# Optimization experiments

Measured on AMD Instinct MI355X. Metric: run time of the kernel, lower is better.

The kernel has to match this reference:

```python
import jax, jax.numpy as jnp
import numpy as np

D_MODEL = 1024
N_HEADS = 8
HEAD_DIM = D_MODEL // N_HEADS
B, T = 4, 2048


def setup_inputs() -> dict:
    key = jax.random.key(0)
    ks = jax.random.split(key, 10)
    x = jax.random.normal(ks[0], (B, T, D_MODEL), dtype=jnp.float32)
    # causal mask: True entries are masked (matches torch masked_fill semantics)
    mask = jnp.triu(jnp.ones((T, T), dtype=bool), k=1)

    def xavier(k, shape):
        fan_in, fan_out = shape[1], shape[0]
        lim = float(np.sqrt(6.0 / (fan_in + fan_out)))
        return jax.random.uniform(k, shape, jnp.float32, -lim, lim)

    Wq = xavier(ks[1], (D_MODEL, D_MODEL)); bq = jnp.zeros((D_MODEL,), jnp.float32)
    Wk = xavier(ks[2], (D_MODEL, D_MODEL)); bk = jnp.zeros((D_MODEL,), jnp.float32)
    Wv = xavier(ks[3], (D_MODEL, D_MODEL)); bv = jnp.zeros((D_MODEL,), jnp.float32)
    Wo = xavier(ks[4], (D_MODEL, D_MODEL)); bo = jnp.zeros((D_MODEL,), jnp.float32)
    return {"x": x, "mask": mask, "Wq": Wq, "bq": bq, "Wk": Wk, "bk": bk,
            "Wv": Wv, "bv": bv, "Wo": Wo, "bo": bo}


def reference(x, mask, Wq, bq, Wk, bk, Wv, bv, Wo, bo):
    Bsz, Tlen, _ = x.shape
    # torch Linear: y = x @ W.T + b
    Q = (x @ Wq.T + bq).reshape(Bsz, Tlen, N_HEADS, HEAD_DIM).transpose(0, 2, 1, 3)  # [B,H,T,Dh]
    K = (x @ Wk.T + bk).reshape(Bsz, Tlen, N_HEADS, HEAD_DIM).transpose(0, 2, 1, 3)  # [B,H,T,Dh]
    V_shared = x @ Wv.T + bv  # [B,T,D] shared across heads
    scale = 1.0 / jnp.sqrt(jnp.float32(HEAD_DIM))
    scores = jnp.einsum('bhqd,bhkd->bhqk', Q, K) * scale  # [B,H,T,T]
    scores = jnp.where(mask[None, None, :, :], jnp.float32(-1e9), scores)
    attn_per_head = jax.nn.softmax(scores, axis=-1)
    alpha_agg = attn_per_head.mean(axis=1)  # [B,T,T] head-averaged attention
    out = jnp.einsum('bqk,bkd->bqd', alpha_agg, V_shared) @ Wo.T + bo
    return out, alpha_agg
```

## Files before the change

kernel.cpp:

```cpp
#include <hip/hip_runtime.h>
#include <hip/hip_bf16.h>

#define D_MODEL 1024
#define NH 8
#define HD 128
#define BATCH 4
#define TSEQ 2048
#define MROWS (BATCH * TSEQ)

typedef __attribute__((ext_vector_type(8))) __bf16 bf16x8;
typedef __attribute__((ext_vector_type(4))) __bf16 bf16x4;
typedef __attribute__((ext_vector_type(4))) float f32x4;
typedef __attribute__((ext_vector_type(8))) unsigned short u16x8;

#define SC2 0.1275174441680632f

__device__ __forceinline__ void gload16(const void* g, void* lds) {
  __builtin_amdgcn_global_load_lds(
      (const __attribute__((address_space(1))) unsigned int*)g,
      (__attribute__((address_space(3))) unsigned int*)lds, 16, 0, 0);
}

__global__ __launch_bounds__(256) void cvt_f32_to_bf16(const float* __restrict__ in,
                                                       __bf16* __restrict__ out, int n4) {
  int i = blockIdx.x * 256 + threadIdx.x;
  if (i < n4) {
    float4 v = reinterpret_cast<const float4*>(in)[i];
    bf16x4 o;
    o[0] = (__bf16)v.x; o[1] = (__bf16)v.y; o[2] = (__bf16)v.z; o[3] = (__bf16)v.w;
    reinterpret_cast<bf16x4*>(out)[i] = o;
  }
}

__global__ __launch_bounds__(256) void cvt4_weights(const float* __restrict__ w0,
                                                    const float* __restrict__ w1,
                                                    const float* __restrict__ w2,
                                                    const float* __restrict__ w3,
                                                    __bf16* __restrict__ out) {
  const int per = D_MODEL * D_MODEL / 4;
  int i = blockIdx.x * 256 + threadIdx.x;
  int m = i / per, j = i - m * per;
  const float* src = (m == 0) ? w0 : (m == 1) ? w1 : (m == 2) ? w2 : w3;
  float4 v = reinterpret_cast<const float4*>(src)[j];
  bf16x4 o;
  o[0] = (__bf16)v.x; o[1] = (__bf16)v.y; o[2] = (__bf16)v.z; o[3] = (__bf16)v.w;
  reinterpret_cast<bf16x4*>(out)[i] = o;
}

template <bool BF16OUT, bool CAUSAL, bool AFP32>
__global__ __launch_bounds__(256) void gemm128(const void* __restrict__ Aip,
                                               const __bf16* __restrict__ Bp,
                                               const float* __restrict__ bias,
                                               void* __restrict__ Yp, int K, int ldy,
                                               size_t sA, size_t sB, size_t sY) {
  __shared__ __bf16 As[2][128 * 32];
  __shared__ __bf16 Bs[2][128 * 32];
  const int tid = threadIdx.x;
  const int w = tid >> 6, l = tid & 63;
  const int lr = l & 15, lg = l >> 4;
  const int m0 = blockIdx.y * 128, n0 = blockIdx.x * 128;
  const int z = blockIdx.z;
  const __bf16* Ab = AFP32 ? nullptr : (const __bf16*)Aip + z * sA;
  const float* Af = AFP32 ? (const float*)Aip + z * sA : nullptr;
  const __bf16* Bb = Bp + z * sB;
  const int wm = w >> 1, wn = w & 1;
  f32x4 acc[4][4] = {};
  const int Klim = CAUSAL ? (m0 + 128 < K ? m0 + 128 : K) : K;
  const int nt = Klim >> 5;

  auto stage = [&](int t, int buf) {
    const int k0 = t << 5;
    if constexpr (!AFP32) {
#pragma unroll
      for (int i = 0; i < 2; ++i) {
        int s = w * 128 + i * 64 + l;
        int row = s >> 2, scp = s & 3;
        int sc = scp ^ ((row >> 1) & 3);
        gload16(Ab + (size_t)(m0 + row) * K + k0 + sc * 8, (char*)As[buf] + s * 16);
      }
    } else {
#pragma unroll
      for (int i = 0; i < 2; ++i) {
        int s = w * 128 + i * 64 + l;
        int row = s >> 2, sc = s & 3;
        const float* src = Af + (size_t)(m0 + row) * K + k0 + sc * 8;
        float4 lo = *reinterpret_cast<const float4*>(src);
        float4 hi = *reinterpret_cast<const float4*>(src + 4);
        bf16x8 v;
        v[0] = (__bf16)lo.x; v[1] = (__bf16)lo.y; v[2] = (__bf16)lo.z; v[3] = (__bf16)lo.w;
        v[4] = (__bf16)hi.x; v[5] = (__bf16)hi.y; v[6] = (__bf16)hi.z; v[7] = (__bf16)hi.w;
        int p = row * 4 + (sc ^ ((row >> 1) & 3));
        *reinterpret_cast<bf16x8*>((char*)As[buf] + p * 16) = v;
      }
    }
#pragma unroll
    for (int i = 0; i < 2; ++i) {
      int s = w * 128 + i * 64 + l;
      int row = s >> 2, scp = s & 3;
      int sc = scp ^ ((row >> 1) & 3);
      gload16(Bb + (size_t)(n0 + row) * K + k0 + sc * 8, (char*)Bs[buf] + s * 16);
    }
  };

  stage(0, 0);
  __syncthreads();
  int cur = 0;
  for (int t = 0; t < nt; ++t) {
    if (t + 1 < nt) stage(t + 1, cur ^ 1);
    bf16x8 af[4], bf[4];
#pragma unroll
    for (int f = 0; f < 4; ++f) {
      int ar = wm * 64 + f * 16 + lr;
      af[f] = *reinterpret_cast<const bf16x8*>((const char*)As[cur] + ar * 64 +
                                               ((lg ^ ((ar >> 1) & 3)) * 16));
      int br = wn * 64 + f * 16 + lr;
      bf[f] = *reinterpret_cast<const bf16x8*>((const char*)Bs[cur] + br * 64 +
                                               ((lg ^ ((br >> 1) & 3)) * 16));
    }
#pragma unroll
    for (int mf = 0; mf < 4; ++mf)
#pragma unroll
      for (int nf = 0; nf < 4; ++nf)
        acc[mf][nf] = __builtin_amdgcn_mfma_f32_16x16x32_bf16(af[mf], bf[nf], acc[mf][nf], 0, 0, 0);
    __syncthreads();
    cur ^= 1;
  }

#pragma unroll
  for (int mf = 0; mf < 4; ++mf) {
#pragma unroll
    for (int nf = 0; nf < 4; ++nf) {
#pragma unroll
      for (int r = 0; r < 4; ++r) {
        int grow = m0 + wm * 64 + mf * 16 + lg * 4 + r;
        int gcol = n0 + wn * 64 + nf * 16 + lr;
        float v = acc[mf][nf][r];
        if (bias) v += bias[gcol];
        if constexpr (BF16OUT)
          ((__bf16*)Yp + z * sY)[(size_t)grow * ldy + gcol] = (__bf16)v;
        else
          ((float*)Yp + z * sY)[(size_t)grow * ldy + gcol] = v;
      }
    }
  }
}

__global__ __launch_bounds__(256) void transpose_v(const __bf16* __restrict__ V,
                                                   __bf16* __restrict__ Vt) {
  __shared__ unsigned short tile[64 * 72];
  const int b = blockIdx.z;
  const int t0 = blockIdx.x * 64, d0 = blockIdx.y * 64;
  const int tid = threadIdx.x;
#pragma unroll
  for (int i = 0; i < 2; ++i) {
    int s = i * 256 + tid;
    int r = s >> 3, c8 = s & 7;
    u16x8 v = *reinterpret_cast<const u16x8*>(V + ((size_t)b * TSEQ + t0 + r) * D_MODEL + d0 + c8 * 8);
    *reinterpret_cast<u16x8*>(&tile[r * 72 + c8 * 8]) = v;
  }
  __syncthreads();
#pragma unroll
  for (int i = 0; i < 2; ++i) {
    int s = i * 256 + tid;
    int dr = s >> 3, t8 = s & 7;
    u16x8 o;
#pragma unroll
    for (int j = 0; j < 8; ++j) o[j] = tile[(t8 * 8 + j) * 72 + dr];
    *reinterpret_cast<u16x8*>(Vt + ((size_t)b * D_MODEL + d0 + dr) * TSEQ + t0 + t8 * 8) = o;
  }
}

#define STAGE_T(srcbase, dst)                                                      \
  {                                                                                \
    _Pragma("unroll") for (int i = 0; i < 4; ++i) {                                \
      int s = i * 256 + tid;                                                       \
      int row = s >> 4, sp = s & 15;                                               \
      int sl = sp ^ (row & 15);                                                    \
      gload16((srcbase) + (size_t)row * D_MODEL + sl * 8, (char*)(dst) + s * 16);  \
    }                                                                              \
  }

__device__ __forceinline__ bf16x8 ldfrag(const __bf16* t, int row, int c, int lg) {
  return *reinterpret_cast<const bf16x8*>((const char*)t + row * 256 +
                                          (((c * 4 + lg) ^ (row & 15)) * 16));
}

__global__ __launch_bounds__(256) void attn_stats(const __bf16* __restrict__ Q,
                                                  const __bf16* __restrict__ Kp,
                                                  float* __restrict__ Linv) {
  __shared__ __bf16 Qs[64 * 128];
  __shared__ __bf16 Ks[2][64 * 128];
  __shared__ float Lred[2][64];
  const int tid = threadIdx.x;
  const int w = tid >> 6, l = tid & 63;
  const int lr = l & 15, lg = l >> 4;
  const int wq = w >> 1, wk = w & 1;
  const int qt = blockIdx.x, q0 = qt * 64;
  const int b = blockIdx.y >> 3, h = blockIdx.y & 7;

  const __bf16* qsrc = Q + ((size_t)(b * TSEQ + q0)) * D_MODEL + h * HD;
  const __bf16* kbase = Kp + ((size_t)b * TSEQ) * D_MODEL + h * HD;
  STAGE_T(qsrc, Qs);
  STAGE_T(kbase, Ks[0]);
  __syncthreads();

  bf16x8 af[2][4];
#pragma unroll
  for (int mf = 0; mf < 2; ++mf)
#pragma unroll
    for (int c = 0; c < 4; ++c) af[mf][c] = ldfrag(Qs, wq * 32 + mf * 16 + lr, c, lg);

  float lsum[2][4] = {};
  int cur = 0;
  for (int kt = 0; kt <= qt; ++kt) {
    if (kt < qt) STAGE_T(kbase + (size_t)(kt + 1) * 64 * D_MODEL, Ks[cur ^ 1]);
    bf16x8 bfr[2][4];
#pragma unroll
    for (int nf = 0; nf < 2; ++nf)
#pragma unroll
      for (int c = 0; c < 4; ++c) bfr[nf][c] = ldfrag(Ks[cur], wk * 32 + nf * 16 + lr, c, lg);
    f32x4 acc[2][2] = {};
#pragma unroll
    for (int c = 0; c < 4; ++c)
#pragma unroll
      for (int mf = 0; mf < 2; ++mf)
#pragma unroll
        for (int nf = 0; nf < 2; ++nf)
          acc[mf][nf] = __builtin_amdgcn_mfma_f32_16x16x32_bf16(af[mf][c], bfr[nf][c], acc[mf][nf], 0, 0, 0);
    if (kt == qt) {
#pragma unroll
      for (int mf = 0; mf < 2; ++mf)
#pragma unroll
        for (int nf = 0; nf < 2; ++nf)
#pragma unroll
          for (int r = 0; r < 4; ++r) {
            int q = q0 + wq * 32 + mf * 16 + lg * 4 + r;
            int k = kt * 64 + wk * 32 + nf * 16 + lr;
            if (k <= q) lsum[mf][r] += exp2f(acc[mf][nf][r] * SC2);
          }
    } else {
#pragma unroll
      for (int mf = 0; mf < 2; ++mf)
#pragma unroll
        for (int nf = 0; nf < 2; ++nf)
#pragma unroll
          for (int r = 0; r < 4; ++r) lsum[mf][r] += exp2f(acc[mf][nf][r] * SC2);
    }
    __syncthreads();
    cur ^= 1;
  }
#pragma unroll
  for (int m = 1; m < 16; m <<= 1)
#pragma unroll
    for (int mf = 0; mf < 2; ++mf)
#pragma unroll
      for (int r = 0; r < 4; ++r) lsum[mf][r] += __shfl_xor(lsum[mf][r], m, 64);
  if (lr == 0) {
#pragma unroll
    for (int mf = 0; mf < 2; ++mf)
#pragma unroll
      for (int r = 0; r < 4; ++r) Lred[wk][wq * 32 + mf * 16 + lg * 4 + r] = lsum[mf][r];
  }
  __syncthreads();
  if (tid < 64) {
    float s = Lred[0][tid] + Lred[1][tid];
    Linv[((size_t)(b * NH + h)) * TSEQ + q0 + tid] = 1.0f / (8.0f * s);
  }
}

__global__ __launch_bounds__(256) void attn_alpha(const __bf16* __restrict__ Q,
                                                  const __bf16* __restrict__ Kp,
                                                  const float* __restrict__ Linv,
                                                  float* __restrict__ alpha) {
  const int kt = blockIdx.x, qt = blockIdx.y, b = blockIdx.z;
  const int q0 = qt * 64, k0 = kt * 64;
  const int tid = threadIdx.x;
  if (kt > qt) {
    float4 zz = {0.f, 0.f, 0.f, 0.f};
#pragma unroll
    for (int i = 0; i < 4; ++i) {
      int s = i * 256 + tid;
      int row = s >> 4, c4 = s & 15;
      *reinterpret_cast<float4*>(alpha + ((size_t)(b * TSEQ) + q0 + row) * TSEQ + k0 + c4 * 4) = zz;
    }
    return;
  }
  __shared__ __bf16 Qs[2][64 * 128];
  __shared__ __bf16 Ks[2][64 * 128];
  const int w = tid >> 6, l = tid & 63;
  const int lr = l & 15, lg = l >> 4;
  const int wq = w >> 1, wk = w & 1;
  const __bf16* qb0 = Q + ((size_t)(b * TSEQ + q0)) * D_MODEL;
  const __bf16* kb0 = Kp + ((size_t)(b * TSEQ + k0)) * D_MODEL;
  float outv[2][2][4] = {};

  STAGE_T(qb0, Qs[0]);
  STAGE_T(kb0, Ks[0]);
  __syncthreads();
  int cur = 0;
  for (int h = 0; h < NH; ++h) {
    if (h + 1 < NH) {
      STAGE_T(qb0 + (h + 1) * HD, Qs[cur ^ 1]);
      STAGE_T(kb0 + (h + 1) * HD, Ks[cur ^ 1]);
    }
    bf16x8 af[2][4], bfr[2][4];
#pragma unroll
    for (int mf = 0; mf < 2; ++mf)
#pragma unroll
      for (int c = 0; c < 4; ++c) af[mf][c] = ldfrag(Qs[cur], wq * 32 + mf * 16 + lr, c, lg);
#pragma unroll
    for (int nf = 0; nf < 2; ++nf)
#pragma unroll
      for (int c = 0; c < 4; ++c) bfr[nf][c] = ldfrag(Ks[cur], wk * 32 + nf * 16 + lr, c, lg);
    f32x4 acc[2][2] = {};
#pragma unroll
    for (int c = 0; c < 4; ++c)
#pragma unroll
      for (int mf = 0; mf < 2; ++mf)
#pragma unroll
        for (int nf = 0; nf < 2; ++nf)
          acc[mf][nf] = __builtin_amdgcn_mfma_f32_16x16x32_bf16(af[mf][c], bfr[nf][c], acc[mf][nf], 0, 0, 0);
    float4 li[2];
#pragma unroll
    for (int mf = 0; mf < 2; ++mf)
      li[mf] = *reinterpret_cast<const float4*>(
          &Linv[((size_t)(b * NH + h)) * TSEQ + q0 + wq * 32 + mf * 16 + lg * 4]);
    if (kt == qt) {
#pragma unroll
      for (int mf = 0; mf < 2; ++mf)
#pragma unroll
        for (int nf = 0; nf < 2; ++nf)
#pragma unroll
          for (int r = 0; r < 4; ++r) {
            int q = q0 + wq * 32 + mf * 16 + lg * 4 + r;
            int k = k0 + wk * 32 + nf * 16 + lr;
            if (k <= q)
              outv[mf][nf][r] += exp2f(acc[mf][nf][r] * SC2) * (&li[mf].x)[r];
          }
    } else {
#pragma unroll
      for (int mf = 0; mf < 2; ++mf)
#pragma unroll
        for (int nf = 0; nf < 2; ++nf)
#pragma unroll
          for (int r = 0; r < 4; ++r)
            outv[mf][nf][r] += exp2f(acc[mf][nf][r] * SC2) * (&li[mf].x)[r];
    }
    __syncthreads();
    cur ^= 1;
  }
#pragma unroll
  for (int mf = 0; mf < 2; ++mf)
#pragma unroll
    for (int nf = 0; nf < 2; ++nf)
#pragma unroll
      for (int r = 0; r < 4; ++r)
        alpha[((size_t)(b * TSEQ) + q0 + wq * 32 + mf * 16 + lg * 4 + r) * TSEQ +
              k0 + wk * 32 + nf * 16 + lr] = outv[mf][nf][r];
}

extern "C" void kernel_launch(void* const* d_in, const int* in_sizes, int n_in,
                              void* d_out, int out_size, void* d_ws, size_t ws_size,
                              hipStream_t stream) {
  const float* x  = (const float*)d_in[0];
  const float* Wq = (const float*)d_in[2];
  const float* bq = (const float*)d_in[3];
  const float* Wk = (const float*)d_in[4];
  const float* bk = (const float*)d_in[5];
  const float* Wv = (const float*)d_in[6];
  const float* bv = (const float*)d_in[7];
  const float* Wo = (const float*)d_in[8];
  const float* bo = (const float*)d_in[9];

  float* out_f = (float*)d_out;
  float* alpha = out_f + (size_t)MROWS * D_MODEL;

  char* p = (char*)d_ws;
  __bf16* xb  = (__bf16*)p; p += (size_t)MROWS * D_MODEL * 2;
  __bf16* wqb = (__bf16*)p; p += (size_t)D_MODEL * D_MODEL * 2;
  __bf16* wkb = (__bf16*)p; p += (size_t)D_MODEL * D_MODEL * 2;
  __bf16* wvb = (__bf16*)p; p += (size_t)D_MODEL * D_MODEL * 2;
  __bf16* wob = (__bf16*)p; p += (size_t)D_MODEL * D_MODEL * 2;
  __bf16* qb  = (__bf16*)p; p += (size_t)MROWS * D_MODEL * 2;
  __bf16* kb  = (__bf16*)p; p += (size_t)MROWS * D_MODEL * 2;
  __bf16* vb  = (__bf16*)p; p += (size_t)MROWS * D_MODEL * 2;
  __bf16* vtb = (__bf16*)p; p += (size_t)BATCH * D_MODEL * TSEQ * 2;
  float* linv = (float*)p;  p += (size_t)BATCH * NH * TSEQ * 4;
  __bf16* midb = xb;

  {
    int n4 = MROWS * D_MODEL / 4;
    cvt_f32_to_bf16<<<n4 / 256, 256, 0, stream>>>(x, xb, n4);
    int w4 = 4 * D_MODEL * D_MODEL / 4;
    cvt4_weights<<<w4 / 256, 256, 0, stream>>>(Wq, Wk, Wv, Wo, wqb);
  }

  dim3 pgrid(D_MODEL / 128, MROWS / 128, 1);
  gemm128<true, false, false><<<pgrid, 256, 0, stream>>>(xb, wqb, bq, qb, D_MODEL, D_MODEL, 0, 0, 0);
  gemm128<true, false, false><<<pgrid, 256, 0, stream>>>(xb, wkb, bk, kb, D_MODEL, D_MODEL, 0, 0, 0);
  gemm128<true, false, false><<<pgrid, 256, 0, stream>>>(xb, wvb, bv, vb, D_MODEL, D_MODEL, 0, 0, 0);

  transpose_v<<<dim3(TSEQ / 64, D_MODEL / 64, BATCH), 256, 0, stream>>>(vb, vtb);

  attn_stats<<<dim3(TSEQ / 64, BATCH * NH), 256, 0, stream>>>(qb, kb, linv);

  attn_alpha<<<dim3(TSEQ / 64, TSEQ / 64, BATCH), 256, 0, stream>>>(qb, kb, linv, alpha);

  gemm128<true, true, true><<<dim3(D_MODEL / 128, TSEQ / 128, BATCH), 256, 0, stream>>>(
      alpha, vtb, nullptr, midb, TSEQ, D_MODEL,
      (size_t)TSEQ * TSEQ, (size_t)D_MODEL * TSEQ, (size_t)TSEQ * D_MODEL);

  gemm128<false, false, false><<<pgrid, 256, 0, stream>>>(midb, wob, bo, out_f, D_MODEL, D_MODEL, 0, 0, 0);
}
```

Baseline: 381.3 us.

## Fuse QKV projection into one GEMM and retile attention to 128x128 blocks

The three Q/K/V projection GEMMs are merged into one GEMM over the contiguous Wq|Wk|Wv bf16 buffer, writing an interleaved [M,3072] QKV tensor with concatenated bias. The row-sum stats kernel becomes a 128x128-tile, 512-thread grid over (k-tile, q-tile, batch) that accumulates per-head exp sums with atomicAdd, followed by a small inversion kernel. The alpha kernel uses the same 128x128 tiling. This cuts launches and raises parallelism and per-block reuse for the stats pass, in exchange for atomics, an extra memset and invert kernel, and more shared memory per block (128 KiB).

New measurement: 393.5 us. 1.03x slower.

```diff
diff --git a/kernel.cpp b/kernel.cpp
--- a/kernel.cpp
+++ b/kernel.cpp
@@ -7,6 +7,7 @@
 #define BATCH 4
 #define TSEQ 2048
 #define MROWS (BATCH * TSEQ)
+#define QKV_LD 3072
 
 typedef __attribute__((ext_vector_type(8))) __bf16 bf16x8;
 typedef __attribute__((ext_vector_type(4))) __bf16 bf16x4;
@@ -45,6 +46,19 @@
   bf16x4 o;
   o[0] = (__bf16)v.x; o[1] = (__bf16)v.y; o[2] = (__bf16)v.z; o[3] = (__bf16)v.w;
   reinterpret_cast<bf16x4*>(out)[i] = o;
+}
+
+__global__ __launch_bounds__(256) void concat_bias(const float* __restrict__ a,
+                                                   const float* __restrict__ b,
+                                                   const float* __restrict__ c,
+                                                   float* __restrict__ o) {
+  int i = blockIdx.x * 256 + threadIdx.x;
+  if (i < 3072) o[i] = (i < 1024) ? a[i] : (i < 2048) ? b[i - 1024] : c[i - 2048];
+}
+
+__global__ __launch_bounds__(256) void invert_lsum(float* __restrict__ L, int n) {
+  int i = blockIdx.x * 256 + threadIdx.x;
+  if (i < n) L[i] = 1.0f / (8.0f * L[i]);
 }
 
 template <bool BF16OUT, bool CAUSAL, bool AFP32>
@@ -155,7 +169,7 @@
   for (int i = 0; i < 2; ++i) {
     int s = i * 256 + tid;
     int r = s >> 3, c8 = s & 7;
-    u16x8 v = *reinterpret_cast<const u16x8*>(V + ((size_t)b * TSEQ + t0 + r) * D_MODEL + d0 + c8 * 8);
+    u16x8 v = *reinterpret_cast<const u16x8*>(V + ((size_t)b * TSEQ + t0 + r) * QKV_LD + d0 + c8 * 8);
     *reinterpret_cast<u16x8*>(&tile[r * 72 + c8 * 8]) = v;
   }
   __syncthreads();
@@ -170,193 +184,136 @@
   }
 }
 
-#define STAGE_T(srcbase, dst)                                                      \
-  {                                                                                \
-    _Pragma("unroll") for (int i = 0; i < 4; ++i) {                                \
-      int s = i * 256 + tid;                                                       \
-      int row = s >> 4, sp = s & 15;                                               \
-      int sl = sp ^ (row & 15);                                                    \
-      gload16((srcbase) + (size_t)row * D_MODEL + sl * 8, (char*)(dst) + s * 16);  \
-    }                                                                              \
-  }
+__device__ __forceinline__ void stage_tile128(const __bf16* __restrict__ src,
+                                              __bf16* __restrict__ dst, int tid, int ld) {
+#pragma unroll
+  for (int i = 0; i < 4; ++i) {
+    int s = i * 512 + tid;
+    int row = s >> 4, sp = s & 15;
+    int sl = sp ^ (row & 15);
+    gload16(src + (size_t)row * ld + sl * 8, (char*)dst + s * 16);
+  }
+}
 
 __device__ __forceinline__ bf16x8 ldfrag(const __bf16* t, int row, int c, int lg) {
   return *reinterpret_cast<const bf16x8*>((const char*)t + row * 256 +
                                           (((c * 4 + lg) ^ (row & 15)) * 16));
 }
 
-__global__ __launch_bounds__(256) void attn_stats(const __bf16* __restrict__ Q,
-                                                  const __bf16* __restrict__ Kp,
-                                                  float* __restrict__ Linv) {
-  __shared__ __bf16 Qs[64 * 128];
-  __shared__ __bf16 Ks[2][64 * 128];
-  __shared__ float Lred[2][64];
+template <int MODE>
+__global__ __launch_bounds__(512) void attn128(const __bf16* __restrict__ QKV,
+                                               const float* __restrict__ Linv,
+                                               float* __restrict__ Out) {
+  const int kt = blockIdx.x, qt = blockIdx.y, b = blockIdx.z;
   const int tid = threadIdx.x;
+  const int q0 = qt * 128, k0 = kt * 128;
+  if (kt > qt) {
+    if (MODE == 1) {
+      float4 zz = {0.f, 0.f, 0.f, 0.f};
+#pragma unroll
+      for (int i = 0; i < 8; ++i) {
+        int s = i * 512 + tid;
+        int row = s >> 5, c = s & 31;
+        *reinterpret_cast<float4*>(Out + ((size_t)(b * TSEQ) + q0 + row) * TSEQ + k0 + c * 4) = zz;
+      }
+    }
+    return;
+  }
+  __shared__ __bf16 Qs[2][128 * 128];
+  __shared__ __bf16 Ks[2][128 * 128];
   const int w = tid >> 6, l = tid & 63;
   const int lr = l & 15, lg = l >> 4;
-  const int wq = w >> 1, wk = w & 1;
-  const int qt = blockIdx.x, q0 = qt * 64;
-  const int b = blockIdx.y >> 3, h = blockIdx.y & 7;
-
-  const __bf16* qsrc = Q + ((size_t)(b * TSEQ + q0)) * D_MODEL + h * HD;
-  const __bf16* kbase = Kp + ((size_t)b * TSEQ) * D_MODEL + h * HD;
-  STAGE_T(qsrc, Qs);
-  STAGE_T(kbase, Ks[0]);
+  const int wq = w >> 1;
+  const int wk = w & 1;
+  const __bf16* qb0 = QKV + (size_t)(b * TSEQ + q0) * QKV_LD;
+  const __bf16* kb0 = QKV + (size_t)(b * TSEQ + k0) * QKV_LD + 1024;
+
+  stage_tile128(qb0, Qs[0], tid, QKV_LD);
+  stage_tile128(kb0, Ks[0], tid, QKV_LD);
   __syncthreads();
 
-  bf16x8 af[2][4];
-#pragma unroll
-  for (int mf = 0; mf < 2; ++mf)
-#pragma unroll
-    for (int c = 0; c < 4; ++c) af[mf][c] = ldfrag(Qs, wq * 32 + mf * 16 + lr, c, lg);
-
-  float lsum[2][4] = {};
-  int cur = 0;
-  for (int kt = 0; kt <= qt; ++kt) {
-    if (kt < qt) STAGE_T(kbase + (size_t)(kt + 1) * 64 * D_MODEL, Ks[cur ^ 1]);
-    bf16x8 bfr[2][4];
-#pragma unroll
-    for (int nf = 0; nf < 2; ++nf)
-#pragma unroll
-      for (int c = 0; c < 4; ++c) bfr[nf][c] = ldfrag(Ks[cur], wk * 32 + nf * 16 + lr, c, lg);
-    f32x4 acc[2][2] = {};
-#pragma unroll
-    for (int c = 0; c < 4; ++c)
-#pragma unroll
-      for (int mf = 0; mf < 2; ++mf)
-#pragma unroll
-        for (int nf = 0; nf < 2; ++nf)
-          acc[mf][nf] = __builtin_amdgcn_mfma_f32_16x16x32_bf16(af[mf][c], bfr[nf][c], acc[mf][nf], 0, 0, 0);
-    if (kt == qt) {
-#pragma unroll
-      for (int mf = 0; mf < 2; ++mf)
-#pragma unroll
-        for (int nf = 0; nf < 2; ++nf)
-#pragma unroll
-          for (int r = 0; r < 4; ++r) {
-            int q = q0 + wq * 32 + mf * 16 + lg * 4 + r;
-            int k = kt * 64 + wk * 32 + nf * 16 + lr;
-            if (k <= q) lsum[mf][r] += exp2f(acc[mf][nf][r] * SC2);
-          }
-    } else {
-#pragma unroll
-      for (int mf = 0; mf < 2; ++mf)
-#pragma unroll
-        for (int nf = 0; nf < 2; ++nf)
-#pragma unroll
-          for (int r = 0; r < 4; ++r) lsum[mf][r] += exp2f(acc[mf][nf][r] * SC2);
-    }
-    __syncthreads();
-    cur ^= 1;
-  }
-#pragma unroll
-  for (int m = 1; m < 16; m <<= 1)
-#pragma unroll
-    for (int mf = 0; mf < 2; ++mf)
-#pragma unroll
-      for (int r = 0; r < 4; ++r) lsum[mf][r] += __shfl_xor(lsum[mf][r], m, 64);
-  if (lr == 0) {
-#pragma unroll
-    for (int mf = 0; mf < 2; ++mf)
-#pragma unroll
-      for (int r = 0; r < 4; ++r) Lred[wk][wq * 32 + mf * 16 + lg * 4 + r] = lsum[mf][r];
-  }
-  __syncthreads();
-  if (tid < 64) {
-    float s = Lred[0][tid] + Lred[1][tid];
-    Linv[((size_t)(b * NH + h)) * TSEQ + q0 + tid] = 1.0f / (8.0f * s);
-  }
-}
-
-__global__ __launch_bounds__(256) void attn_alpha(const __bf16* __restrict__ Q,
-                                                  const __bf16* __restrict__ Kp,
-                                                  const float* __restrict__ Linv,
-                                                  float* __restrict__ alpha) {
-  const int kt = blockIdx.x, qt = blockIdx.y, b = blockIdx.z;
-  const int q0 = qt * 64, k0 = kt * 64;
-  const int tid = threadIdx.x;
-  if (kt > qt) {
-    float4 zz = {0.f, 0.f, 0.f, 0.f};
-#pragma unroll
-    for (int i = 0; i < 4; ++i) {
-      int s = i * 256 + tid;
-      int row = s >> 4, c4 = s & 15;
-      *reinterpret_cast<float4*>(alpha + ((size_t)(b * TSEQ) + q0 + row) * TSEQ + k0 + c4 * 4) = zz;
-    }
-    return;
-  }
-  __shared__ __bf16 Qs[2][64 * 128];
-  __shared__ __bf16 Ks[2][64 * 128];
-  const int w = tid >> 6, l = tid & 63;
-  const int lr = l & 15, lg = l >> 4;
-  const int wq = w >> 1, wk = w & 1;
-  const __bf16* qb0 = Q + ((size_t)(b * TSEQ + q0)) * D_MODEL;
-  const __bf16* kb0 = Kp + ((size_t)(b * TSEQ + k0)) * D_MODEL;
-  float outv[2][2][4] = {};
-
-  STAGE_T(qb0, Qs[0]);
-  STAGE_T(kb0, Ks[0]);
-  __syncthreads();
+  float outv[2][4][4] = {};
   int cur = 0;
   for (int h = 0; h < NH; ++h) {
     if (h + 1 < NH) {
-      STAGE_T(qb0 + (h + 1) * HD, Qs[cur ^ 1]);
-      STAGE_T(kb0 + (h + 1) * HD, Ks[cur ^ 1]);
-    }
-    bf16x8 af[2][4], bfr[2][4];
+      stage_tile128(qb0 + (h + 1) * HD, Qs[cur ^ 1], tid, QKV_LD);
+      stage_tile128(kb0 + (h + 1) * HD, Ks[cur ^ 1], tid, QKV_LD);
+    }
+    bf16x8 af[2][4], bf[4][4];
 #pragma unroll
     for (int mf = 0; mf < 2; ++mf)
 #pragma unroll
       for (int c = 0; c < 4; ++c) af[mf][c] = ldfrag(Qs[cur], wq * 32 + mf * 16 + lr, c, lg);
 #pragma unroll
-    for (int nf = 0; nf < 2; ++nf)
-#pragma unroll
-      for (int c = 0; c < 4; ++c) bfr[nf][c] = ldfrag(Ks[cur], wk * 32 + nf * 16 + lr, c, lg);
-    f32x4 acc[2][2] = {};
+    for (int nf = 0; nf < 4; ++nf)
+#pragma unroll
+      for (int c = 0; c < 4; ++c) bf[nf][c] = ldfrag(Ks[cur], wk * 64 + nf * 16 + lr, c, lg);
+    f32x4 acc[2][4] = {};
 #pragma unroll
     for (int c = 0; c < 4; ++c)
 #pragma unroll
       for (int mf = 0; mf < 2; ++mf)
 #pragma unroll
-        for (int nf = 0; nf < 2; ++nf)
-          acc[mf][nf] = __builtin_amdgcn_mfma_f32_16x16x32_bf16(af[mf][c], bfr[nf][c], acc[mf][nf], 0, 0, 0);
-    float4 li[2];
-#pragma unroll
-    for (int mf = 0; mf < 2; ++mf)
-      li[mf] = *reinterpret_cast<const float4*>(
-          &Linv[((size_t)(b * NH + h)) * TSEQ + q0 + wq * 32 + mf * 16 + lg * 4]);
-    if (kt == qt) {
+        for (int nf = 0; nf < 4; ++nf)
+          acc[mf][nf] = __builtin_amdgcn_mfma_f32_16x16x32_bf16(af[mf][c], bf[nf][c], acc[mf][nf], 0, 0, 0);
+
+    if constexpr (MODE == 0) {
+      float ls[2][4] = {};
 #pragma unroll
       for (int mf = 0; mf < 2; ++mf)
 #pragma unroll
-        for (int nf = 0; nf < 2; ++nf)
+        for (int nf = 0; nf < 4; ++nf)
 #pragma unroll
           for (int r = 0; r < 4; ++r) {
             int q = q0 + wq * 32 + mf * 16 + lg * 4 + r;
-            int k = k0 + wk * 32 + nf * 16 + lr;
-            if (k <= q)
+            int k = k0 + wk * 64 + nf * 16 + lr;
+            if (kt < qt || k <= q) ls[mf][r] += exp2f(acc[mf][nf][r] * SC2);
+          }
+#pragma unroll
+      for (int m = 1; m < 16; m <<= 1)
+#pragma unroll
+        for (int mf = 0; mf < 2; ++mf)
+#pragma unroll
+          for (int r = 0; r < 4; ++r) ls[mf][r] += __shfl_xor(ls[mf][r], m, 64);
+      if (lr == 0) {
+#pragma unroll
+        for (int mf = 0; mf < 2; ++mf)
+#pragma unroll
+          for (int r = 0; r < 4; ++r)
+            atomicAdd(&Out[((size_t)(b * NH + h)) * TSEQ + q0 + wq * 32 + mf * 16 + lg * 4 + r],
+                      ls[mf][r]);
+      }
+    } else {
+      float4 li[2];
+#pragma unroll
+      for (int mf = 0; mf < 2; ++mf)
+        li[mf] = *reinterpret_cast<const float4*>(
+            &Linv[((size_t)(b * NH + h)) * TSEQ + q0 + wq * 32 + mf * 16 + lg * 4]);
+#pragma unroll
+      for (int mf = 0; mf < 2; ++mf)
+#pragma unroll
+        for (int nf = 0; nf < 4; ++nf)
+#pragma unroll
+          for (int r = 0; r < 4; ++r) {
+            int q = q0 + wq * 32 + mf * 16 + lg * 4 + r;
+            int k = k0 + wk * 64 + nf * 16 + lr;
+            if (kt < qt || k <= q)
               outv[mf][nf][r] += exp2f(acc[mf][nf][r] * SC2) * (&li[mf].x)[r];
           }
-    } else {
-#pragma unroll
-      for (int mf = 0; mf < 2; ++mf)
-#pragma unroll
-        for (int nf = 0; nf < 2; ++nf)
-#pragma unroll
-          for (int r = 0; r < 4; ++r)
-            outv[mf][nf][r] += exp2f(acc[mf][nf][r] * SC2) * (&li[mf].x)[r];
     }
     __syncthreads();
     cur ^= 1;
   }
-#pragma unroll
-  for (int mf = 0; mf < 2; ++mf)
-#pragma unroll
-    for (int nf = 0; nf < 2; ++nf)
-#pragma unroll
-      for (int r = 0; r < 4; ++r)
-        alpha[((size_t)(b * TSEQ) + q0 + wq * 32 + mf * 16 + lg * 4 + r) * TSEQ +
-              k0 + wk * 32 + nf * 16 + lr] = outv[mf][nf][r];
+  if constexpr (MODE == 1) {
+#pragma unroll
+    for (int mf = 0; mf < 2; ++mf)
+#pragma unroll
+      for (int nf = 0; nf < 4; ++nf)
+#pragma unroll
+        for (int r = 0; r < 4; ++r)
+          Out[((size_t)(b * TSEQ) + q0 + wq * 32 + mf * 16 + lg * 4 + r) * TSEQ +
+              k0 + wk * 64 + nf * 16 + lr] = outv[mf][nf][r];
+  }
 }
 
 extern "C" void kernel_launch(void* const* d_in, const int* in_sizes, int n_in,
@@ -376,39 +333,41 @@
   float* alpha = out_f + (size_t)MROWS * D_MODEL;
 
   char* p = (char*)d_ws;
-  __bf16* xb  = (__bf16*)p; p += (size_t)MROWS * D_MODEL * 2;
-  __bf16* wqb = (__bf16*)p; p += (size_t)D_MODEL * D_MODEL * 2;
-  __bf16* wkb = (__bf16*)p; p += (size_t)D_MODEL * D_MODEL * 2;
-  __bf16* wvb = (__bf16*)p; p += (size_t)D_MODEL * D_MODEL * 2;
-  __bf16* wob = (__bf16*)p; p += (size_t)D_MODEL * D_MODEL * 2;
-  __bf16* qb  = (__bf16*)p; p += (size_t)MROWS * D_MODEL * 2;
-  __bf16* kb  = (__bf16*)p; p += (size_t)MROWS * D_MODEL * 2;
-  __bf16* vb  = (__bf16*)p; p += (size_t)MROWS * D_MODEL * 2;
-  __bf16* vtb = (__bf16*)p; p += (size_t)BATCH * D_MODEL * TSEQ * 2;
-  float* linv = (float*)p;  p += (size_t)BATCH * NH * TSEQ * 4;
+  __bf16* xb   = (__bf16*)p; p += (size_t)MROWS * D_MODEL * 2;
+  __bf16* wqb  = (__bf16*)p; p += (size_t)D_MODEL * D_MODEL * 2;
+  __bf16* wkb  = (__bf16*)p; p += (size_t)D_MODEL * D_MODEL * 2;
+  __bf16* wvb  = (__bf16*)p; p += (size_t)D_MODEL * D_MODEL * 2;
+  __bf16* wob  = (__bf16*)p; p += (size_t)D_MODEL * D_MODEL * 2;
+  __bf16* qkv  = (__bf16*)p; p += (size_t)MROWS * QKV_LD * 2;
+  __bf16* vtb  = (__bf16*)p; p += (size_t)BATCH * D_MODEL * TSEQ * 2;
+  float* lsum  = (float*)p;  p += (size_t)BATCH * NH * TSEQ * 4;
+  float* bcat  = (float*)p;  p += 3072 * 4;
   __bf16* midb = xb;
+
+  hipMemsetAsync(lsum, 0, (size_t)BATCH * NH * TSEQ * 4, stream);
 
   {
     int n4 = MROWS * D_MODEL / 4;
     cvt_f32_to_bf16<<<n4 / 256, 256, 0, stream>>>(x, xb, n4);
     int w4 = 4 * D_MODEL * D_MODEL / 4;
     cvt4_weights<<<w4 / 256, 256, 0, stream>>>(Wq, Wk, Wv, Wo, wqb);
-  }
-
-  dim3 pgrid(D_MODEL / 128, MROWS / 128, 1);
-  gemm128<true, false, false><<<pgrid, 256, 0, stream>>>(xb, wqb, bq, qb, D_MODEL, D_MODEL, 0, 0, 0);
-  gemm128<true, false, false><<<pgrid, 256, 0, stream>>>(xb, wkb, bk, kb, D_MODEL, D_MODEL, 0, 0, 0);
-  gemm128<true, false, false><<<pgrid, 256, 0, stream>>>(xb, wvb, bv, vb, D_MODEL, D_MODEL, 0, 0, 0);
-
-  transpose_v<<<dim3(TSEQ / 64, D_MODEL / 64, BATCH), 256, 0, stream>>>(vb, vtb);
-
-  attn_stats<<<dim3(TSEQ / 64, BATCH * NH), 256, 0, stream>>>(qb, kb, linv);
-
-  attn_alpha<<<dim3(TSEQ / 64, TSEQ / 64, BATCH), 256, 0, stream>>>(qb, kb, linv, alpha);
+    concat_bias<<<12, 256, 0, stream>>>(bq, bk, bv, bcat);
+  }
+
+  gemm128<true, false, false><<<dim3(QKV_LD / 128, MROWS / 128), 256, 0, stream>>>(
+      xb, wqb, bcat, qkv, D_MODEL, QKV_LD, 0, 0, 0);
+
+  transpose_v<<<dim3(TSEQ / 64, D_MODEL / 64, BATCH), 256, 0, stream>>>(qkv + 2048, vtb);
+
+  attn128<0><<<dim3(TSEQ / 128, TSEQ / 128, BATCH), 512, 0, stream>>>(qkv, nullptr, lsum);
+  invert_lsum<<<(BATCH * NH * TSEQ) / 256, 256, 0, stream>>>(lsum, BATCH * NH * TSEQ);
+
+  attn128<1><<<dim3(TSEQ / 128, TSEQ / 128, BATCH), 512, 0, stream>>>(qkv, lsum, alpha);
 
   gemm128<true, true, true><<<dim3(D_MODEL / 128, TSEQ / 128, BATCH), 256, 0, stream>>>(
       alpha, vtb, nullptr, midb, TSEQ, D_MODEL,
       (size_t)TSEQ * TSEQ, (size_t)D_MODEL * TSEQ, (size_t)TSEQ * D_MODEL);
 
-  gemm128<false, false, false><<<pgrid, 256, 0, stream>>>(midb, wob, bo, out_f, D_MODEL, D_MODEL, 0, 0, 0);
-}
+  gemm128<false, false, false><<<dim3(D_MODEL / 128, MROWS / 128), 256, 0, stream>>>(
+      midb, wob, bo, out_f, D_MODEL, D_MODEL, 0, 0, 0);
+}
```
